# Kernel tuning notes

Hardware: AMD Instinct MI355X
Metric: run time of the kernel (lower is better)

Reference implementation:

```python
import jax, jax.numpy as jnp
import numpy as np

D_MODEL = 1024
NUM_HEADS = 16
HEAD_DIM = D_MODEL // NUM_HEADS
CAUSAL = True


def rope_cos_sin(seq_len, dim):
    inv_freq = 1.0 / (10000.0 ** (jnp.arange(0, dim, 2, dtype=jnp.float32) / dim))
    t = jnp.arange(seq_len, dtype=jnp.float32)
    freqs = jnp.einsum('i,j->ij', t, inv_freq)          # [S, dim/2]
    emb = jnp.concatenate([freqs, freqs], axis=-1)      # [S, dim]
    return jnp.cos(emb), jnp.sin(emb)


def rotate_half(x):
    x1, x2 = jnp.split(x, 2, axis=-1)
    return jnp.concatenate([-x2, x1], axis=-1)


def setup_inputs() -> dict:
    key = jax.random.key(0)
    k1, k2, k3, k4, k5 = jax.random.split(key, 5)
    B, S = 2, 2048
    x = jax.random.normal(k1, (B, S, D_MODEL), dtype=jnp.float32)
    s = 1.0 / np.sqrt(D_MODEL)
    W_qkv = jax.random.normal(k2, (D_MODEL, 3 * D_MODEL), dtype=jnp.float32) * s
    b_qkv = jax.random.normal(k3, (3 * D_MODEL,), dtype=jnp.float32) * 0.01
    W_out = jax.random.normal(k4, (D_MODEL, D_MODEL), dtype=jnp.float32) * s
    b_out = jax.random.normal(k5, (D_MODEL,), dtype=jnp.float32) * 0.01
    return {"x": x, "W_qkv": W_qkv, "b_qkv": b_qkv, "W_out": W_out, "b_out": b_out}


def reference(x, W_qkv, b_qkv, W_out, b_out):
    B, S, _ = x.shape
    qkv = x @ W_qkv + b_qkv                              # [B, S, 3D]
    q, k, v = jnp.split(qkv, 3, axis=-1)
    # [B, H, S, hd]
    q = q.reshape(B, S, NUM_HEADS, HEAD_DIM).transpose(0, 2, 1, 3)
    k = k.reshape(B, S, NUM_HEADS, HEAD_DIM).transpose(0, 2, 1, 3)
    v = v.reshape(B, S, NUM_HEADS, HEAD_DIM).transpose(0, 2, 1, 3)
    cos, sin = rope_cos_sin(S, HEAD_DIM)                 # [S, hd]
    cos = cos[None, None]
    sin = sin[None, None]
    q = q * cos + rotate_half(q) * sin
    k = k * cos + rotate_half(k) * sin
    scores = jnp.einsum('bhqd,bhkd->bhqk', q, k) / np.sqrt(HEAD_DIM)
    if CAUSAL:
        causal_mask = jnp.triu(jnp.ones((S, S), dtype=bool), k=1)
        scores = jnp.where(causal_mask, -jnp.inf, scores)
    attn = jax.nn.softmax(scores, axis=-1)
    out = jnp.einsum('bhqk,bhkd->bhqd', attn, v)         # [B, H, S, hd]
    out = out.transpose(0, 2, 1, 3).reshape(B, S, D_MODEL)
    return out @ W_out + b_out
```

## Files before the change

### kernel.cpp

```cpp
#include <hip/hip_runtime.h>
#include <hip/hip_bf16.h>
#include <math.h>

typedef __bf16 bf16;
typedef __bf16 bf16x8 __attribute__((ext_vector_type(8)));
typedef unsigned short ushort8 __attribute__((ext_vector_type(8)));
typedef float floatx4 __attribute__((ext_vector_type(4)));

#define MFMA_BF16(a, b, c) __builtin_amdgcn_mfma_f32_16x16x32_bf16(a, b, c, 0, 0, 0)

#define Q_SCALE 0.18033688011112042f
#define NEG_INVFREQ_LOG2 0.41524101186092029f
#define INV_2PI 0.15915494309189535f

#if __has_builtin(__builtin_amdgcn_exp2f)
#define EXP2F(x) __builtin_amdgcn_exp2f(x)
#else
#define EXP2F(x) exp2f(x)
#endif

__device__ __forceinline__ void hw_sincos_rev(float rev, float* sn, float* cs) {
#if __has_builtin(__builtin_amdgcn_sinf) && __has_builtin(__builtin_amdgcn_cosf) && \
    __has_builtin(__builtin_amdgcn_fractf)
  const float f = __builtin_amdgcn_fractf(rev);
  *sn = __builtin_amdgcn_sinf(f);
  *cs = __builtin_amdgcn_cosf(f);
#else
  sincosf(rev * 6.2831853071795864f, sn, cs);
#endif
}

__device__ __forceinline__ bf16x8 cvt8(const float4 a, const float4 b) {
  bf16x8 t;
  t[0] = (bf16)a.x; t[1] = (bf16)a.y; t[2] = (bf16)a.z; t[3] = (bf16)a.w;
  t[4] = (bf16)b.x; t[5] = (bf16)b.y; t[6] = (bf16)b.z; t[7] = (bf16)b.w;
  return t;
}

__device__ __forceinline__ unsigned int pack2(float a, float b) {
#if __has_builtin(__builtin_amdgcn_cvt_pk_bf16_f32)
  return __builtin_bit_cast(unsigned int, __builtin_amdgcn_cvt_pk_bf16_f32(a, b));
#else
  unsigned short lo = __builtin_bit_cast(unsigned short, (bf16)a);
  unsigned short hi = __builtin_bit_cast(unsigned short, (bf16)b);
  return (unsigned int)lo | ((unsigned int)hi << 16);
#endif
}

__device__ __forceinline__ void gld16(const bf16* g, bf16* l) {
  __builtin_amdgcn_global_load_lds(
      (const __attribute__((address_space(1))) unsigned int*)g,
      (__attribute__((address_space(3))) unsigned int*)l, 16, 0, 0);
}

__global__ __launch_bounds__(256) void cast_x_kernel(const float* __restrict__ in,
                                                     bf16* __restrict__ out) {
  const int i = blockIdx.x * 256 + threadIdx.x;
  const float4 a = *(const float4*)&in[(size_t)i * 8];
  const float4 b = *(const float4*)&in[(size_t)i * 8 + 4];
  *(bf16x8*)&out[(size_t)i * 8] = cvt8(a, b);
}

__global__ __launch_bounds__(256) void transpose_w_kernel(
    const float* __restrict__ in, bf16* __restrict__ out, int N, int K) {
  __shared__ __align__(16) bf16 T[64][40];
  const int t = threadIdx.x;
  const int k0 = blockIdx.y * 32, n0 = blockIdx.x * 64;
  {
    const int k = t >> 3, n8 = (t & 7) * 8;
    const float* p = &in[(size_t)(k0 + k) * N + n0 + n8];
    const float4 a = *(const float4*)p;
    const float4 b = *(const float4*)(p + 4);
    const float v[8] = {a.x, a.y, a.z, a.w, b.x, b.y, b.z, b.w};
#pragma unroll
    for (int j = 0; j < 8; j++) {
      const int n = n8 + j;
      T[n][k ^ (8 * ((n >> 3) & 3))] = (bf16)v[j];
    }
  }
  __syncthreads();
  {
    const int n = t >> 2, k8 = (t & 3) * 8;
    const int kp = k8 ^ (8 * ((n >> 3) & 3));
    *(bf16x8*)&out[(size_t)(n0 + n) * K + k0 + k8] = *(const bf16x8*)&T[n][kp];
  }
}

template <int TN, int MODE>
__global__ __launch_bounds__(256) void gemm_kernel(
    const bf16* __restrict__ A, const bf16* __restrict__ Bt,
    const float* __restrict__ bias, void* __restrict__ out0,
    bf16* __restrict__ outK, bf16* __restrict__ outV, int M, int N, int K) {
  constexpr int NI = TN / 32;
  constexpr int BI = TN / 32;
  __shared__ __align__(16) bf16 As2[2][128][32];
  __shared__ __align__(16) bf16 Bs2[2][TN][32];

  const int tid = threadIdx.x, lane = tid & 63, w = tid >> 6;
  const int c = lane & 15, quad = lane >> 4;
  const int wm = w >> 1, wn = w & 1;
  const int m0 = blockIdx.y * 128, n0 = blockIdx.x * TN;
  const int srow = lane >> 2, scol = (lane & 3) * 8;

  floatx4 acc[4][NI] = {};

  for (int k0 = 0; k0 < K; k0 += 64) {
    __syncthreads();
#pragma unroll
    for (int i = 0; i < 4; i++) {
      const int seg = w * 4 + i;
      const int kh = seg >> 3, r0 = (seg & 7) * 16;
      gld16(&A[(size_t)(m0 + r0 + srow) * K + k0 + kh * 32 + scol],
            &As2[kh][r0][0]);
    }
#pragma unroll
    for (int i = 0; i < BI; i++) {
      const int seg = w * BI + i;
      const int kh = seg / (TN / 16), r0 = (seg % (TN / 16)) * 16;
      gld16(&Bt[(size_t)(n0 + r0 + srow) * K + k0 + kh * 32 + scol],
            &Bs2[kh][r0][0]);
    }
    __syncthreads();

#pragma unroll
    for (int kh = 0; kh < 2; kh++) {
      bf16x8 af[4], bfr[NI];
#pragma unroll
      for (int mi = 0; mi < 4; mi++)
        af[mi] = *(const bf16x8*)&As2[kh][wm * 64 + mi * 16 + c][quad * 8];
#pragma unroll
      for (int ni = 0; ni < NI; ni++)
        bfr[ni] = *(const bf16x8*)&Bs2[kh][wn * (TN / 2) + ni * 16 + c][quad * 8];
#pragma unroll
      for (int mi = 0; mi < 4; mi++)
#pragma unroll
        for (int ni = 0; ni < NI; ni++)
          acc[mi][ni] = MFMA_BF16(af[mi], bfr[ni], acc[mi][ni]);
    }
  }

  if (MODE == 0) {
#pragma unroll
    for (int mi = 0; mi < 4; mi++)
#pragma unroll
      for (int ni = 0; ni < NI; ni++)
#pragma unroll
        for (int r = 0; r < 4; r++) {
          const int row = m0 + wm * 64 + mi * 16 + quad * 4 + r;
          const int col = n0 + wn * (TN / 2) + ni * 16 + c;
          ((float*)out0)[(size_t)row * N + col] = acc[mi][ni][r] + bias[col];
        }
  } else {
    const int colb = n0 + wn * (TN / 2);
    const int t = colb >> 10;
    const int h = (colb & 1023) >> 6;
    bf16* dst = (t == 0) ? (bf16*)out0 : (t == 1 ? outK : outV);
    if (t == 2) {
#pragma unroll
      for (int mi = 0; mi < 4; mi++)
#pragma unroll
        for (int ni = 0; ni < NI; ni++)
#pragma unroll
          for (int r = 0; r < 4; r++) {
            const int row = m0 + wm * 64 + mi * 16 + quad * 4 + r;
            const int col = colb + ni * 16 + c;
            const int b = row >> 11, s = row & 2047;
            dst[(((size_t)b * 16 + h) * 2048 + s) * 64 + (col & 63)] =
                (bf16)(acc[mi][ni][r] + bias[col]);
          }
    } else {
      const float qs = (t == 0) ? Q_SCALE : 1.0f;
      const float invr[2] = {exp2f(-NEG_INVFREQ_LOG2 * (float)c) * INV_2PI,
                             exp2f(-NEG_INVFREQ_LOG2 * (float)(16 + c)) * INV_2PI};
#pragma unroll
      for (int mi = 0; mi < 4; mi++) {
#pragma unroll
        for (int r = 0; r < 4; r++) {
          const int row = m0 + wm * 64 + mi * 16 + quad * 4 + r;
          const int b = row >> 11, s = row & 2047;
          const size_t base = (((size_t)b * 16 + h) * 2048 + s) * 64;
#pragma unroll
          for (int ni = 0; ni < 2; ni++) {
            float sn, cs;
            hw_sincos_rev((float)s * invr[ni], &sn, &cs);
            const float v1 = acc[mi][ni][r] + bias[colb + ni * 16 + c];
            const float v2 = acc[mi][ni + 2][r] + bias[colb + (ni + 2) * 16 + c];
            const int d = ni * 16 + c;
            dst[base + d] = (bf16)((v1 * cs - v2 * sn) * qs);
            dst[base + d + 32] = (bf16)((v2 * cs + v1 * sn) * qs);
          }
        }
      }
    }
  }
}

struct AttnState {
  floatx4 o[4];
  floatx4 l;
};

__device__ __forceinline__ void attn_step(
    const bf16x8 qf[2], const bf16x8 kf[4][2], const bf16x8 vf[4][2],
    const bf16x8 ones, bf16 (*PsW)[72], AttnState& st, int qglob, int kbase,
    bool diag, int c, int quad) {
  floatx4 sacc[4] = {};
#pragma unroll
  for (int kg = 0; kg < 4; kg++)
#pragma unroll
    for (int dh = 0; dh < 2; dh++)
      sacc[kg] = MFMA_BF16(kf[kg][dh], qf[dh], sacc[kg]);

#pragma unroll
  for (int kg = 0; kg < 4; kg++) {
    float p[4];
#pragma unroll
    for (int r = 0; r < 4; r++) {
      float e = EXP2F(sacc[kg][r]);
      if (diag && (kbase + kg * 16 + quad * 4 + r > qglob)) e = 0.0f;
      p[r] = e;
    }
    const uint2 u = {pack2(p[0], p[1]), pack2(p[2], p[3])};
    *(uint2*)&PsW[c][kg * 16 + quad * 4] = u;
  }

  bf16x8 pf[2];
#pragma unroll
  for (int ks = 0; ks < 2; ks++)
    pf[ks] = *(const bf16x8*)&PsW[c][ks * 32 + quad * 8];

#pragma unroll
  for (int dg = 0; dg < 4; dg++)
#pragma unroll
    for (int ks = 0; ks < 2; ks++)
      st.o[dg] = MFMA_BF16(vf[dg][ks], pf[ks], st.o[dg]);
  st.l = MFMA_BF16(ones, pf[0], st.l);
  st.l = MFMA_BF16(ones, pf[1], st.l);
}

__global__ __launch_bounds__(256) void attn_kernel(const bf16* __restrict__ Q,
                                                   const bf16* __restrict__ K,
                                                   const bf16* __restrict__ V,
                                                   bf16* __restrict__ Aout) {
  const int S = 2048;
  const int bh = blockIdx.y;
  const int p = blockIdx.x;
  const int tid = threadIdx.x, lane = tid & 63, wave = tid >> 6;
  const int c = lane & 15, quad = lane >> 4;

  __shared__ __align__(16) bf16 Ks2[2][2][64][32];
  __shared__ __align__(16) bf16 Vt[2][64][72];
  __shared__ __align__(16) bf16 Ps[4][2][16][72];

  const bf16* Qb = Q + (size_t)bh * S * 64;
  const bf16* Kb = K + (size_t)bh * S * 64;
  const bf16* Vb = V + (size_t)bh * S * 64;
  const int b = bh >> 4, h = bh & 15;

  const int qA = p, qB = 31 - p;
  const int qgA = qA * 64 + wave * 16 + c;
  const int qgB = qB * 64 + wave * 16 + c;

  bf16x8 qfA[2], qfB[2];
#pragma unroll
  for (int dh = 0; dh < 2; dh++) {
    qfA[dh] = *(const bf16x8*)&Qb[(size_t)qgA * 64 + dh * 32 + quad * 8];
    qfB[dh] = *(const bf16x8*)&Qb[(size_t)qgB * 64 + dh * 32 + quad * 8];
  }

  bf16x8 ones;
#pragma unroll
  for (int j = 0; j < 8; j++) ones[j] = (bf16)1.0f;

  AttnState stA = {}, stB = {};

  const int vcc = (tid & 7) * 8;
  const int vr2 = ((tid >> 3) + 4 * (tid & 7)) & 31;
  const int ksr = lane >> 2, ksc = (lane & 3) * 8;

  {
#pragma unroll
    for (int i = 0; i < 2; i++) {
      const int seg = wave * 2 + i;
      const int dh = seg >> 2, r0 = (seg & 3) * 16;
      gld16(&Kb[(size_t)(r0 + ksr) * 64 + dh * 32 + ksc], &Ks2[0][dh][r0][0]);
    }
    const bf16* vs = &Vb[(size_t)(2 * vr2) * 64 + vcc];
    const ushort8 w0 = __builtin_bit_cast(ushort8, *(const bf16x8*)vs);
    const ushort8 w1 = __builtin_bit_cast(ushort8, *(const bf16x8*)(vs + 64));
#pragma unroll
    for (int j = 0; j < 8; j++)
      *(unsigned int*)&Vt[0][vcc + j][2 * vr2] =
          (unsigned int)w0[j] | ((unsigned int)w1[j] << 16);
  }
  __syncthreads();

  int buf = 0;
  for (int kt = 0; kt <= qB; kt++) {
    const bool pfetch = (kt < qB);
    ushort8 nw0, nw1;
    if (pfetch) {
      const bf16* vs = &Vb[(size_t)((kt + 1) * 64 + 2 * vr2) * 64 + vcc];
      nw0 = __builtin_bit_cast(ushort8, *(const bf16x8*)vs);
      nw1 = __builtin_bit_cast(ushort8, *(const bf16x8*)(vs + 64));
#pragma unroll
      for (int i = 0; i < 2; i++) {
        const int seg = wave * 2 + i;
        const int dh = seg >> 2, r0 = (seg & 3) * 16;
        gld16(&Kb[(size_t)((kt + 1) * 64 + r0 + ksr) * 64 + dh * 32 + ksc],
              &Ks2[buf ^ 1][dh][r0][0]);
      }
    }

    bf16x8 kf[4][2];
#pragma unroll
    for (int kg = 0; kg < 4; kg++)
#pragma unroll
      for (int dh = 0; dh < 2; dh++)
        kf[kg][dh] = *(const bf16x8*)&Ks2[buf][dh][kg * 16 + c][quad * 8];

    bf16x8 vf[4][2];
#pragma unroll
    for (int dg = 0; dg < 4; dg++)
#pragma unroll
      for (int ks = 0; ks < 2; ks++)
        vf[dg][ks] = *(const bf16x8*)&Vt[buf][dg * 16 + c][ks * 32 + quad * 8];

    attn_step(qfB, kf, vf, ones, Ps[wave][0], stB, qgB, kt * 64, kt == qB, c,
              quad);
    if (kt <= qA)
      attn_step(qfA, kf, vf, ones, Ps[wave][1], stA, qgA, kt * 64, kt == qA, c,
                quad);

    if (pfetch) {
#pragma unroll
      for (int j = 0; j < 8; j++)
        *(unsigned int*)&Vt[buf ^ 1][vcc + j][2 * vr2] =
            (unsigned int)nw0[j] | ((unsigned int)nw1[j] << 16);
    }
    __syncthreads();
    buf ^= 1;
  }

  const float ivA = 1.0f / stA.l[0], ivB = 1.0f / stB.l[0];

#pragma unroll
  for (int dg = 0; dg < 4; dg++) {
    const uint2 uA = {pack2(stA.o[dg][0] * ivA, stA.o[dg][1] * ivA),
                      pack2(stA.o[dg][2] * ivA, stA.o[dg][3] * ivA)};
    const uint2 uB = {pack2(stB.o[dg][0] * ivB, stB.o[dg][1] * ivB),
                      pack2(stB.o[dg][2] * ivB, stB.o[dg][3] * ivB)};
    *(uint2*)&Aout[((size_t)b * 2048 + qgA) * 1024 + h * 64 + dg * 16 + quad * 4] = uA;
    *(uint2*)&Aout[((size_t)b * 2048 + qgB) * 1024 + h * 64 + dg * 16 + quad * 4] = uB;
  }
}

extern "C" void kernel_launch(void* const* d_in, const int* in_sizes, int n_in,
                              void* d_out, int out_size, void* d_ws,
                              size_t ws_size, hipStream_t stream) {
  const float* x = (const float*)d_in[0];
  const float* W_qkv = (const float*)d_in[1];
  const float* b_qkv = (const float*)d_in[2];
  const float* W_out = (const float*)d_in[3];
  const float* b_out = (const float*)d_in[4];
  float* out = (float*)d_out;

  const int B = 2, S = 2048, NH = 16;
  const size_t qn = (size_t)B * NH * S * 64;

  bf16* xb = (bf16*)d_ws;
  bf16* Wqkvt = xb + qn;
  bf16* Wot = Wqkvt + 3072 * 1024;
  bf16* Qw = Wot + 1024 * 1024;
  bf16* Kw = Qw + qn;
  bf16* Vw = Kw + qn;
  bf16* AO = xb;

  cast_x_kernel<<<dim3(qn / 8 / 256), 256, 0, stream>>>(x, xb);
  transpose_w_kernel<<<dim3(3072 / 64, 1024 / 32), 256, 0, stream>>>(
      W_qkv, Wqkvt, 3072, 1024);
  transpose_w_kernel<<<dim3(1024 / 64, 1024 / 32), 256, 0, stream>>>(
      W_out, Wot, 1024, 1024);

  gemm_kernel<128, 1><<<dim3(3072 / 128, 4096 / 128), 256, 0, stream>>>(
      xb, Wqkvt, b_qkv, Qw, Kw, Vw, 4096, 3072, 1024);
  attn_kernel<<<dim3(16, B * NH), 256, 0, stream>>>(Qw, Kw, Vw, AO);
  gemm_kernel<64, 0><<<dim3(1024 / 64, 4096 / 128), 256, 0, stream>>>(
      AO, Wot, b_out, out, nullptr, nullptr, 4096, 1024, 1024);
}
```

Measured before the change: 193.5 us.

## Store V pre-transposed from QKV GEMM and async-load it with swizzled LDS

Result: no change. 191.8 us (-0.9%).

```diff
diff --git a/kernel.cpp b/kernel.cpp
--- a/kernel.cpp
+++ b/kernel.cpp
@@ -157,17 +157,18 @@
     bf16* dst = (t == 0) ? (bf16*)out0 : (t == 1 ? outK : outV);
     if (t == 2) {
 #pragma unroll
-      for (int mi = 0; mi < 4; mi++)
-#pragma unroll
-        for (int ni = 0; ni < NI; ni++)
-#pragma unroll
-          for (int r = 0; r < 4; r++) {
-            const int row = m0 + wm * 64 + mi * 16 + quad * 4 + r;
-            const int col = colb + ni * 16 + c;
-            const int b = row >> 11, s = row & 2047;
-            dst[(((size_t)b * 16 + h) * 2048 + s) * 64 + (col & 63)] =
-                (bf16)(acc[mi][ni][r] + bias[col]);
-          }
+      for (int ni = 0; ni < NI; ni++) {
+        const int d = ni * 16 + c;
+        const float bv = bias[colb + ni * 16 + c];
+#pragma unroll
+        for (int mi = 0; mi < 4; mi++) {
+          const int row = m0 + wm * 64 + mi * 16 + quad * 4;
+          const int b = row >> 11, s = row & 2047;
+          const uint2 u = {pack2(acc[mi][ni][0] + bv, acc[mi][ni][1] + bv),
+                           pack2(acc[mi][ni][2] + bv, acc[mi][ni][3] + bv)};
+          *(uint2*)&dst[(((size_t)b * 16 + h) * 64 + d) * 2048 + s] = u;
+        }
+      }
     } else {
       const float qs = (t == 0) ? Q_SCALE : 1.0f;
       const float invr[2] = {exp2f(-NEG_INVFREQ_LOG2 * (float)c) * INV_2PI,
@@ -249,7 +250,7 @@
   const int c = lane & 15, quad = lane >> 4;
 
   __shared__ __align__(16) bf16 Ks2[2][2][64][32];
-  __shared__ __align__(16) bf16 Vt[2][64][72];
+  __shared__ __align__(16) bf16 Vt[2][64][64];
   __shared__ __align__(16) bf16 Ps[4][2][16][72];
 
   const bf16* Qb = Q + (size_t)bh * S * 64;
@@ -274,43 +275,34 @@
 
   AttnState stA = {}, stB = {};
 
-  const int vcc = (tid & 7) * 8;
-  const int vr2 = ((tid >> 3) + 4 * (tid & 7)) & 31;
   const int ksr = lane >> 2, ksc = (lane & 3) * 8;
-
-  {
+  const int vd = lane >> 3;
+  const int vg = lane & 7;
+
+  auto stage = [&](int bb, int kt) {
+    const int kt64 = kt * 64;
 #pragma unroll
     for (int i = 0; i < 2; i++) {
       const int seg = wave * 2 + i;
       const int dh = seg >> 2, r0 = (seg & 3) * 16;
-      gld16(&Kb[(size_t)(r0 + ksr) * 64 + dh * 32 + ksc], &Ks2[0][dh][r0][0]);
-    }
-    const bf16* vs = &Vb[(size_t)(2 * vr2) * 64 + vcc];
-    const ushort8 w0 = __builtin_bit_cast(ushort8, *(const bf16x8*)vs);
-    const ushort8 w1 = __builtin_bit_cast(ushort8, *(const bf16x8*)(vs + 64));
-#pragma unroll
-    for (int j = 0; j < 8; j++)
-      *(unsigned int*)&Vt[0][vcc + j][2 * vr2] =
-          (unsigned int)w0[j] | ((unsigned int)w1[j] << 16);
-  }
+      gld16(&Kb[(size_t)(kt64 + r0 + ksr) * 64 + dh * 32 + ksc],
+            &Ks2[bb][dh][r0][0]);
+    }
+#pragma unroll
+    for (int i = 0; i < 2; i++) {
+      const int d0 = wave * 16 + i * 8;
+      const int dd = d0 + vd;
+      const int g = vg ^ (dd & 7);
+      gld16(&Vb[(size_t)dd * 2048 + kt64 + g * 8], &Vt[bb][d0][0]);
+    }
+  };
+
+  stage(0, 0);
   __syncthreads();
 
   int buf = 0;
   for (int kt = 0; kt <= qB; kt++) {
-    const bool pfetch = (kt < qB);
-    ushort8 nw0, nw1;
-    if (pfetch) {
-      const bf16* vs = &Vb[(size_t)((kt + 1) * 64 + 2 * vr2) * 64 + vcc];
-      nw0 = __builtin_bit_cast(ushort8, *(const bf16x8*)vs);
-      nw1 = __builtin_bit_cast(ushort8, *(const bf16x8*)(vs + 64));
-#pragma unroll
-      for (int i = 0; i < 2; i++) {
-        const int seg = wave * 2 + i;
-        const int dh = seg >> 2, r0 = (seg & 3) * 16;
-        gld16(&Kb[(size_t)((kt + 1) * 64 + r0 + ksr) * 64 + dh * 32 + ksc],
-              &Ks2[buf ^ 1][dh][r0][0]);
-      }
-    }
+    if (kt < qB) stage(buf ^ 1, kt + 1);
 
     bf16x8 kf[4][2];
 #pragma unroll
@@ -321,10 +313,14 @@
 
     bf16x8 vf[4][2];
 #pragma unroll
-    for (int dg = 0; dg < 4; dg++)
-#pragma unroll
-      for (int ks = 0; ks < 2; ks++)
-        vf[dg][ks] = *(const bf16x8*)&Vt[buf][dg * 16 + c][ks * 32 + quad * 8];
+    for (int dg = 0; dg < 4; dg++) {
+      const int d = dg * 16 + c;
+#pragma unroll
+      for (int ks = 0; ks < 2; ks++) {
+        const int g = (ks * 4 + quad) ^ (c & 7);
+        vf[dg][ks] = *(const bf16x8*)&Vt[buf][d][g * 8];
+      }
+    }
 
     attn_step(qfB, kf, vf, ones, Ps[wave][0], stB, qgB, kt * 64, kt == qB, c,
               quad);
@@ -332,12 +328,6 @@
       attn_step(qfA, kf, vf, ones, Ps[wave][1], stA, qgA, kt * 64, kt == qA, c,
                 quad);
 
-    if (pfetch) {
-#pragma unroll
-      for (int j = 0; j < 8; j++)
-        *(unsigned int*)&Vt[buf ^ 1][vcc + j][2 * vr2] =
-            (unsigned int)nw0[j] | ((unsigned int)nw1[j] << 16);
-    }
     __syncthreads();
     buf ^= 1;
   }
```
